# Optimization experiments

Hardware: AMD Instinct MI355X
Metric: run time of the kernel (lower is better)

The kernel has to match this reference:

```python
import jax, jax.numpy as jnp
import numpy as np

B, S, D, H, HID = 4, 2048, 1024, 16, 4096
DK = D // H
EPS = 1e-6


def layernorm(x, alpha, bias):
    # Matches the custom LayerNorm: std with Bessel correction (torch default),
    # and eps added to std (not variance).
    mean = jnp.mean(x, axis=-1, keepdims=True)
    std = jnp.std(x, axis=-1, ddof=1, keepdims=True)
    return alpha * (x - mean) / (std + EPS) + bias


def setup_inputs() -> dict:
    key = jax.random.key(0)
    ks = jax.random.split(key, 10)
    s = 0.02
    return {
        "x": jax.random.normal(ks[0], (B, S, D), dtype=jnp.float32),
        "wq": jax.random.normal(ks[1], (D, D), dtype=jnp.float32) * s,
        "wk": jax.random.normal(ks[2], (D, D), dtype=jnp.float32) * s,
        "wv": jax.random.normal(ks[3], (D, D), dtype=jnp.float32) * s,
        "wo": jax.random.normal(ks[4], (D, D), dtype=jnp.float32) * s,
        "w1": jax.random.normal(ks[5], (D, HID), dtype=jnp.float32) * s,
        "b1": jnp.zeros((HID,), dtype=jnp.float32),
        "w2": jax.random.normal(ks[6], (HID, D), dtype=jnp.float32) * s,
        "b2": jnp.zeros((D,), dtype=jnp.float32),
        "ln1_a": jnp.ones((D,), dtype=jnp.float32),
        "ln1_b": jnp.zeros((D,), dtype=jnp.float32),
        "ln2_a": jnp.ones((D,), dtype=jnp.float32),
        "ln2_b": jnp.zeros((D,), dtype=jnp.float32),
    }


def reference(x, wq, wk, wv, wo, w1, b1, w2, b2, ln1_a, ln1_b, ln2_a, ln2_b):
    # --- residual 1: pre-norm self-attention ---
    h = layernorm(x, ln1_a, ln1_b)
    q = (h @ wq).reshape(B, S, H, DK)
    k = (h @ wk).reshape(B, S, H, DK)
    v = (h @ wv).reshape(B, S, H, DK)
    scores = jnp.einsum("bqhd,bkhd->bhqk", q, k) / jnp.sqrt(jnp.float32(DK))
    # Faithful replication of the original mask: tril on a (1, max_len) matrix
    # keeps only key position 0; all other key positions get -1e9.
    key_keep = (jnp.arange(S) == 0)  # [S]
    scores = jnp.where(key_keep[None, None, None, :], scores, jnp.float32(-1e9))
    attn = jax.nn.softmax(scores, axis=-1)  # [B,H,S,S]
    ctx = jnp.einsum("bhqk,bkhd->bqhd", attn, v).reshape(B, S, D)
    x = x + ctx @ wo
    # --- residual 2: pre-norm FFN ---
    h2 = layernorm(x, ln2_a, ln2_b)
    ff = jax.nn.gelu(h2 @ w1 + b1, approximate=False) @ w2 + b2
    return x + ff
```

## Files before the change

kernel.cpp:

```cpp
#include <hip/hip_runtime.h>
#include <cstdint>

#define D_MODEL 1024
#define HIDDEN  4096
#define BATCH   4
#define SEQ     2048
#define NROWS   (BATCH*SEQ)

typedef __attribute__((ext_vector_type(4))) int i32x4;

#define ACT_AMAX 4.0f
#define ACT_S    (ACT_AMAX / 127.0f)
#define ACT_INV  (127.0f / ACT_AMAX)

#define GLDS16(g, l) __builtin_amdgcn_global_load_lds(                        \
    (const __attribute__((address_space(1))) unsigned int*)(g),               \
    (__attribute__((address_space(3))) unsigned int*)(l), 16, 0, 0)

__device__ __forceinline__ float block_sum(float v, float* s4) {
  #pragma unroll
  for (int off = 32; off > 0; off >>= 1) v += __shfl_down(v, off);
  int lane = threadIdx.x & 63, wid = threadIdx.x >> 6;
  __syncthreads();
  if (lane == 0) s4[wid] = v;
  __syncthreads();
  return s4[0] + s4[1] + s4[2] + s4[3];
}

__device__ __forceinline__ float block_max(float v, float* s4) {
  #pragma unroll
  for (int off = 32; off > 0; off >>= 1) v = fmaxf(v, __shfl_down(v, off));
  int lane = threadIdx.x & 63, wid = threadIdx.x >> 6;
  __syncthreads();
  if (lane == 0) s4[wid] = v;
  __syncthreads();
  return fmaxf(fmaxf(s4[0], s4[1]), fmaxf(s4[2], s4[3]));
}

__device__ __forceinline__ signed char qclamp(float v) {
  float r = rintf(v);
  r = fminf(127.f, fmaxf(-127.f, r));
  return (signed char)(int)r;
}

#define KCHUNKS 32
#define KCH     (D_MODEL / KCHUNKS)


__device__ __forceinline__ void absmax_cols_body(
    const float* __restrict__ in, int R, int C, unsigned* __restrict__ u,
    int bx, int by) {
  int c  = bx * 256 + threadIdx.x;
  int r0 = by * 64;
  float m = 0.f;
  #pragma unroll 4
  for (int r = 0; r < 64; ++r)
    m = fmaxf(m, fabsf(in[(size_t)(r0 + r) * C + c]));
  atomicMax(&u[c], __float_as_uint(m));
}

__device__ __forceinline__ void transpose_quant_body(
    const float* __restrict__ in, signed char* __restrict__ out,
    int R, int C, const unsigned* __restrict__ u,
    float (*tile)[33], int bx, int by) {
  int c0 = bx * 32, r0 = by * 32;
  int tx = threadIdx.x & 31, ty = threadIdx.x >> 5;
  #pragma unroll
  for (int i = ty; i < 32; i += 8)
    tile[i][tx] = in[(size_t)(r0 + i) * C + c0 + tx];
  __syncthreads();
  #pragma unroll
  for (int i = ty; i < 32; i += 8) {
    float f = __uint_as_float(u[c0 + i]);
    float inv = f > 0.f ? 127.f / f : 0.f;
    out[(size_t)(c0 + i) * R + r0 + tx] = qclamp(tile[tx][i] * inv);
  }
}

__device__ __forceinline__ void ln_matvec_body(
    const float* __restrict__ x, const float* __restrict__ ln_a,
    const float* __restrict__ ln_b, const float* __restrict__ W,
    float* __restrict__ vout, float* s4, float (*hs)[KCH], int bx, int by) {
  int n  = bx * 256 + threadIdx.x;
  int k0 = by * KCH;
  int t  = threadIdx.x;
  float4 g4 = ((const float4*)ln_a)[t];
  float4 b4 = ((const float4*)ln_b)[t];
  #pragma unroll
  for (int b = 0; b < 4; ++b) {
    const float* xr = x + (size_t)b * SEQ * D_MODEL;
    float4 v = ((const float4*)xr)[t];
    float sum = v.x + v.y + v.z + v.w;
    float mean = block_sum(sum, s4) * (1.f / 1024.f);
    float cx = v.x - mean, cy = v.y - mean, cz = v.z - mean, cw = v.w - mean;
    float sq = cx * cx + cy * cy + cz * cz + cw * cw;
    float var = block_sum(sq, s4) * (1.f / 1023.f);
    float inv = 1.f / (sqrtf(var) + 1e-6f);
    if (t >= (k0 >> 2) && t < ((k0 + KCH) >> 2)) {
      int lc = 4 * t - k0;
      hs[b][lc + 0] = g4.x * cx * inv + b4.x;
      hs[b][lc + 1] = g4.y * cy * inv + b4.y;
      hs[b][lc + 2] = g4.z * cz * inv + b4.z;
      hs[b][lc + 3] = g4.w * cw * inv + b4.w;
    }
  }
  __syncthreads();
  float a0 = 0, a1 = 0, a2 = 0, a3 = 0;
  #pragma unroll
  for (int k = 0; k < KCH; ++k) {
    float w = W[(size_t)(k0 + k) * D_MODEL + n];
    a0 = fmaf(hs[0][k], w, a0);
    a1 = fmaf(hs[1][k], w, a1);
    a2 = fmaf(hs[2][k], w, a2);
    a3 = fmaf(hs[3][k], w, a3);
  }
  atomicAdd(&vout[0 * D_MODEL + n], a0);
  atomicAdd(&vout[1 * D_MODEL + n], a1);
  atomicAdd(&vout[2 * D_MODEL + n], a2);
  atomicAdd(&vout[3 * D_MODEL + n], a3);
}

__device__ __forceinline__ void matvec_body(
    const float* __restrict__ vin, const float* __restrict__ W,
    float* __restrict__ vout, float (*hs)[KCH], int bx, int by) {
  int n  = bx * 256 + threadIdx.x;
  int k0 = by * KCH;
  if (threadIdx.x < 4 * KCH)
    hs[threadIdx.x / KCH][threadIdx.x % KCH] =
        vin[(threadIdx.x / KCH) * D_MODEL + k0 + (threadIdx.x % KCH)];
  __syncthreads();
  float a0 = 0, a1 = 0, a2 = 0, a3 = 0;
  #pragma unroll
  for (int k = 0; k < KCH; ++k) {
    float w = W[(size_t)(k0 + k) * D_MODEL + n];
    a0 = fmaf(hs[0][k], w, a0);
    a1 = fmaf(hs[1][k], w, a1);
    a2 = fmaf(hs[2][k], w, a2);
    a3 = fmaf(hs[3][k], w, a3);
  }
  atomicAdd(&vout[0 * D_MODEL + n], a0);
  atomicAdd(&vout[1 * D_MODEL + n], a1);
  atomicAdd(&vout[2 * D_MODEL + n], a2);
  atomicAdd(&vout[3 * D_MODEL + n], a3);
}

__global__ __launch_bounds__(256) void pre1(
    const float* __restrict__ w1, const float* __restrict__ w2,
    unsigned* __restrict__ u1, unsigned* __restrict__ u2,
    const float* __restrict__ x, const float* __restrict__ ln1a,
    const float* __restrict__ ln1b, const float* __restrict__ wv,
    float* __restrict__ v0) {
  __shared__ float s4[4];
  __shared__ float hs[4][KCH];
  int id = blockIdx.x;
  if (id < 256) {
    absmax_cols_body(w1, D_MODEL, HIDDEN, u1, id & 15, id >> 4);
  } else if (id < 512) {
    int r = id - 256;
    absmax_cols_body(w2, HIDDEN, D_MODEL, u2, r & 3, r >> 2);
  } else {
    int r = id - 512;
    ln_matvec_body(x, ln1a, ln1b, wv, v0, s4, hs, r & 3, r >> 2);
  }
}

__global__ __launch_bounds__(256) void pre2(
    const float* __restrict__ w1, const float* __restrict__ w2,
    const unsigned* __restrict__ u1, const unsigned* __restrict__ u2,
    signed char* __restrict__ w1t, signed char* __restrict__ w2t,
    const float* __restrict__ v0, const float* __restrict__ wo,
    float* __restrict__ delta) {
  __shared__ float tile[32][33];
  __shared__ float hs[4][KCH];
  int id = blockIdx.x;
  if (id < 4096) {
    transpose_quant_body(w1, w1t, D_MODEL, HIDDEN, u1, tile, id & 127, id >> 7);
  } else if (id < 8192) {
    int r = id - 4096;
    transpose_quant_body(w2, w2t, HIDDEN, D_MODEL, u2, tile, r & 31, r >> 5);
  } else {
    int r = id - 8192;
    matvec_body(v0, wo, delta, hs, r & 3, r >> 2);
  }
}

__global__ __launch_bounds__(256) void fused_res_ln_q(
    const float* __restrict__ x, const float* __restrict__ delta,
    const float* __restrict__ g, const float* __restrict__ be,
    float* __restrict__ x1_out, signed char* __restrict__ h2,
    float* __restrict__ hscale) {
  __shared__ float s4[4];
  int row = blockIdx.x;
  int b = row >> 11;
  int t = threadIdx.x;
  float4 v  = ((const float4*)(x + (size_t)row * D_MODEL))[t];
  float4 d4 = ((const float4*)(delta + (size_t)b * D_MODEL))[t];
  v.x += d4.x; v.y += d4.y; v.z += d4.z; v.w += d4.w;
  float sum = v.x + v.y + v.z + v.w;
  float mean = block_sum(sum, s4) * (1.f / 1024.f);
  float cx = v.x - mean, cy = v.y - mean, cz = v.z - mean, cw = v.w - mean;
  float sq = cx * cx + cy * cy + cz * cz + cw * cw;
  float var = block_sum(sq, s4) * (1.f / 1023.f);
  float inv = 1.f / (sqrtf(var) + 1e-6f);
  ((float4*)(x1_out + (size_t)row * D_MODEL))[t] = v;
  float4 g4 = ((const float4*)g)[t];
  float4 b4 = ((const float4*)be)[t];
  float h0v = g4.x * cx * inv + b4.x;
  float h1v = g4.y * cy * inv + b4.y;
  float h2v = g4.z * cz * inv + b4.z;
  float h3v = g4.w * cw * inv + b4.w;
  float am = fmaxf(fmaxf(fabsf(h0v), fabsf(h1v)), fmaxf(fabsf(h2v), fabsf(h3v)));
  float amax = block_max(am, s4);
  float qs = amax > 0.f ? 127.f / amax : 0.f;
  unsigned q = ((unsigned)(unsigned char)(int)qclamp(h0v * qs)) |
               ((unsigned)(unsigned char)(int)qclamp(h1v * qs) << 8) |
               ((unsigned)(unsigned char)(int)qclamp(h2v * qs) << 16) |
               ((unsigned)(unsigned char)(int)qclamp(h3v * qs) << 24);
  ((unsigned*)(h2 + (size_t)row * D_MODEL))[t] = q;
  if (t == 0) hscale[row] = amax * (1.f / 127.f);
}

__global__ __launch_bounds__(256, 3) void gemm1_k128(
    const signed char* __restrict__ A, const signed char* __restrict__ Bt,
    const float* __restrict__ rowS, const unsigned* __restrict__ colU,
    const float* __restrict__ bias, signed char* __restrict__ Cq,
    int M, int N, int K) {
  __shared__ signed char LA[128][128];
  __shared__ signed char LB[128][128];

  int GN  = N / 128;
  int CX  = (GN >= 16) ? 16 : (GN >> 1);
  int id  = blockIdx.x;
  int xcd = id & 7;
  int r   = id >> 3;
  int cby = xcd >> 1, cbx = xcd & 1;
  int lby = r / CX,   lbx = r % CX;
  int by  = cby * 16 + lby;
  int bx  = cbx * CX + lbx;
  int m0  = by * 128, n0 = bx * 128;
  int NT  = K / 128;

  int t = threadIdx.x;
  int wid = t >> 6, lane = t & 63;
  int wm = wid >> 1, wn = wid & 1;
  int lr = lane & 15, kg = lane >> 4;
  int swz = (lr & 7) << 4;

  int rS = t >> 3;
  int cS = ((t & 7) ^ (rS & 7)) * 16;
  const signed char* Ag = A  + (size_t)(m0 + rS) * K + cS;
  const signed char* Bg = Bt + (size_t)(n0 + rS) * K + cS;
  int ldsOff = wid * 1024;

#define G1_STG(T) do {                                                         \
    size_t ko_ = (size_t)(T) * 128;                                            \
    GLDS16(Ag + ko_,                  &LA[0][0] + ldsOff);                     \
    GLDS16(Ag + ko_ + (size_t)32 * K, &LA[0][0] + ldsOff + 4096);              \
    GLDS16(Ag + ko_ + (size_t)64 * K, &LA[0][0] + ldsOff + 8192);              \
    GLDS16(Ag + ko_ + (size_t)96 * K, &LA[0][0] + ldsOff + 12288);             \
    GLDS16(Bg + ko_,                  &LB[0][0] + ldsOff);                     \
    GLDS16(Bg + ko_ + (size_t)32 * K, &LB[0][0] + ldsOff + 4096);              \
    GLDS16(Bg + ko_ + (size_t)64 * K, &LB[0][0] + ldsOff + 8192);              \
    GLDS16(Bg + ko_ + (size_t)96 * K, &LB[0][0] + ldsOff + 12288);             \
  } while (0)

#define G1_RD() do {                                                           \
    _Pragma("unroll") for (int mi = 0; mi < 4; ++mi)                           \
    _Pragma("unroll") for (int kk = 0; kk < 2; ++kk)                           \
      a[mi][kk] = *(const i32x4*)                                              \
          &LA[wm * 64 + mi * 16 + lr][(kk * 64 + kg * 16) ^ swz];              \
    _Pragma("unroll") for (int ni = 0; ni < 4; ++ni)                           \
    _Pragma("unroll") for (int kk = 0; kk < 2; ++kk)                           \
      b[ni][kk] = *(const i32x4*)                                              \
          &LB[wn * 64 + ni * 16 + lr][(kk * 64 + kg * 16) ^ swz];              \
  } while (0)

#define G1_MM() do {                                                           \
    _Pragma("unroll") for (int mi = 0; mi < 4; ++mi)                           \
    _Pragma("unroll") for (int ni = 0; ni < 4; ++ni)                           \
    _Pragma("unroll") for (int kk = 0; kk < 2; ++kk)                           \
      acc[mi][ni] = __builtin_amdgcn_mfma_i32_16x16x64_i8(                     \
          a[mi][kk], b[ni][kk], acc[mi][ni], 0, 0, 0);                         \
  } while (0)

  i32x4 acc[4][4] = {};
  i32x4 a[4][2];
  i32x4 b[4][2];

  for (int tt = 0; tt < NT; ++tt) {
    G1_STG(tt);
    asm volatile("s_waitcnt vmcnt(0)" ::: "memory");
    __builtin_amdgcn_s_barrier();
    G1_RD();
    G1_MM();
    __builtin_amdgcn_s_barrier();
  }

  int orow = m0 + wm * 64;
  int ocol = n0 + wn * 64;
  #pragma unroll
  for (int mf = 0; mf < 4; ++mf) {
    #pragma unroll
    for (int nf = 0; nf < 4; ++nf) {
      int col = ocol + nf * 16 + lr;
      float cs = __uint_as_float(colU[col]) * (1.f / 127.f);
      float bz = bias[col];
      #pragma unroll
      for (int j = 0; j < 4; ++j) {
        int row = orow + mf * 16 + kg * 4 + j;
        float rs = rowS[row];
        float val = (float)acc[mf][nf][j] * rs * cs + bz;
        float u = val * (0.7978845608f + 0.0356774081f * val * val);
        float e = __expf(2.f * u);
        float th = 1.f - 2.f / (e + 1.f);
        val = 0.5f * val * (1.f + th);
        Cq[(size_t)row * N + col] = qclamp(val * ACT_INV);
      }
    }
  }
#undef G1_STG
#undef G1_RD
#undef G1_MM
}

__global__ __launch_bounds__(256, 2) void gemm2_k256(
    const signed char* __restrict__ A, const signed char* __restrict__ Bt,
    const unsigned* __restrict__ colU, const float* __restrict__ bias,
    float* __restrict__ Cf, int M, int N, int K) {
  __shared__ signed char LA[128][256];
  __shared__ signed char LB[128][256];

  int GN  = N / 128;
  int CX  = (GN >= 16) ? 16 : (GN >> 1);
  int id  = blockIdx.x;
  int xcd = id & 7;
  int r   = id >> 3;
  int cby = xcd >> 1, cbx = xcd & 1;
  int lby = r / CX,   lbx = r % CX;
  int by  = cby * 16 + lby;
  int bx  = cbx * CX + lbx;
  int m0  = by * 128, n0 = bx * 128;
  int NT  = K / 256;

  int t = threadIdx.x;
  int wid = t >> 6, lane = t & 63;
  int wm = wid >> 1, wn = wid & 1;
  int lr = lane & 15, kg = lane >> 4;
  int swz = (lr & 7) << 4;

  int rS = t >> 4;
  int cS = ((t & 15) ^ (rS & 7)) * 16;
  const signed char* Ag = A  + (size_t)(m0 + rS) * K + cS;
  const signed char* Bg = Bt + (size_t)(n0 + rS) * K + cS;
  int ldsOff = wid * 1024;

#define G2_STG(T) do {                                                         \
    size_t ko_ = (size_t)(T) * 256;                                            \
    _Pragma("unroll") for (int j = 0; j < 8; ++j)                              \
      GLDS16(Ag + ko_ + (size_t)(16 * j) * K,                                  \
             &LA[0][0] + ldsOff + j * 4096);                                   \
    _Pragma("unroll") for (int j = 0; j < 8; ++j)                              \
      GLDS16(Bg + ko_ + (size_t)(16 * j) * K,                                  \
             &LB[0][0] + ldsOff + j * 4096);                                   \
  } while (0)

#define G2_RD() do {                                                           \
    _Pragma("unroll") for (int mi = 0; mi < 4; ++mi)                           \
    _Pragma("unroll") for (int kk = 0; kk < 4; ++kk)                           \
      a[mi][kk] = *(const i32x4*)                                              \
          &LA[wm * 64 + mi * 16 + lr][(kk * 64 + kg * 16) ^ swz];              \
    _Pragma("unroll") for (int ni = 0; ni < 4; ++ni)                           \
    _Pragma("unroll") for (int kk = 0; kk < 4; ++kk)                           \
      b[ni][kk] = *(const i32x4*)                                              \
          &LB[wn * 64 + ni * 16 + lr][(kk * 64 + kg * 16) ^ swz];              \
  } while (0)

#define G2_MM() do {                                                           \
    _Pragma("unroll") for (int mi = 0; mi < 4; ++mi)                           \
    _Pragma("unroll") for (int ni = 0; ni < 4; ++ni)                           \
    _Pragma("unroll") for (int kk = 0; kk < 4; ++kk)                           \
      acc[mi][ni] = __builtin_amdgcn_mfma_i32_16x16x64_i8(                     \
          a[mi][kk], b[ni][kk], acc[mi][ni], 0, 0, 0);                         \
  } while (0)

  i32x4 acc[4][4] = {};
  i32x4 a[4][4];
  i32x4 b[4][4];

  for (int tt = 0; tt < NT; ++tt) {
    G2_STG(tt);
    asm volatile("s_waitcnt vmcnt(0)" ::: "memory");
    __builtin_amdgcn_s_barrier();
    G2_RD();
    G2_MM();
    __builtin_amdgcn_s_barrier();
  }

  int orow = m0 + wm * 64;
  int ocol = n0 + wn * 64;
  #pragma unroll
  for (int mf = 0; mf < 4; ++mf) {
    #pragma unroll
    for (int nf = 0; nf < 4; ++nf) {
      int col = ocol + nf * 16 + lr;
      float cs = __uint_as_float(colU[col]) * (1.f / 127.f);
      float bz = bias[col];
      #pragma unroll
      for (int j = 0; j < 4; ++j) {
        int row = orow + mf * 16 + kg * 4 + j;
        float val = (float)acc[mf][nf][j] * ACT_S * cs + bz;
        size_t idx = (size_t)row * N + col;
        Cf[idx] = Cf[idx] + val;
      }
    }
  }
#undef G2_STG
#undef G2_RD
#undef G2_MM
}

extern "C" void kernel_launch(void* const* d_in, const int* in_sizes, int n_in,
                              void* d_out, int out_size, void* d_ws, size_t ws_size,
                              hipStream_t stream) {
  const float* x    = (const float*)d_in[0];
  const float* wv   = (const float*)d_in[3];
  const float* wo   = (const float*)d_in[4];
  const float* w1   = (const float*)d_in[5];
  const float* b1   = (const float*)d_in[6];
  const float* w2   = (const float*)d_in[7];
  const float* b2   = (const float*)d_in[8];
  const float* ln1a = (const float*)d_in[9];
  const float* ln1b = (const float*)d_in[10];
  const float* ln2a = (const float*)d_in[11];
  const float* ln2b = (const float*)d_in[12];
  float* out = (float*)d_out;

  char* ws = (char*)d_ws;
  signed char* w1t = (signed char*)(ws);
  signed char* w2t = (signed char*)(ws + (4ull  << 20));
  signed char* h2  = (signed char*)(ws + (8ull  << 20));
  signed char* act = (signed char*)(ws + (16ull << 20));
  char* sc = ws + (48ull << 20);
  unsigned* u1    = (unsigned*)(sc);
  unsigned* u2    = (unsigned*)(sc + 16384);
  float*    v0    = (float*)(sc + 20480);
  float*    delta = (float*)(sc + 36864);
  float*    hsc   = (float*)(sc + 53248);

  hipMemsetAsync(sc, 0, 53248, stream);

  pre1<<<640, 256, 0, stream>>>(w1, w2, u1, u2, x, ln1a, ln1b, wv, v0);

  pre2<<<8320, 256, 0, stream>>>(w1, w2, u1, u2, w1t, w2t, v0, wo, delta);

  fused_res_ln_q<<<NROWS, 256, 0, stream>>>(x, delta, ln2a, ln2b, out, h2, hsc);

  gemm1_k128<<<(NROWS / 128) * (HIDDEN / 128), 256, 0, stream>>>(
      h2, w1t, hsc, u1, b1, act, NROWS, HIDDEN, D_MODEL);

  gemm2_k256<<<(NROWS / 128) * (D_MODEL / 128), 256, 0, stream>>>(
      act, w2t, u2, b2, out, NROWS, D_MODEL, HIDDEN);
}
```

Measured before the change: 167.6 us.

## Double-buffer LDS tiles in both int8 FFN GEMMs to overlap loads with MFMA

Both int8 GEMMs now hold two LDS stages and prefetch the next K tile with global_load_lds while MFMAs run on the current one. A partial vmcnt wait lets the newer loads stay in flight across the barrier. gemm2 drops its K tile from 256 to 128 so two stages fit in the same LDS footprint. gemm1's occupancy hint goes from 3 to 2 blocks per CU because its LDS use doubles, and the last iteration issues a redundant reload of the final tile.

```diff
diff --git a/kernel.cpp b/kernel.cpp
--- a/kernel.cpp
+++ b/kernel.cpp
@@ -220,13 +220,13 @@
   if (t == 0) hscale[row] = amax * (1.f / 127.f);
 }
 
-__global__ __launch_bounds__(256, 3) void gemm1_k128(
+__global__ __launch_bounds__(256, 2) void gemm1_t4(
     const signed char* __restrict__ A, const signed char* __restrict__ Bt,
     const float* __restrict__ rowS, const unsigned* __restrict__ colU,
     const float* __restrict__ bias, signed char* __restrict__ Cq,
     int M, int N, int K) {
-  __shared__ signed char LA[128][128];
-  __shared__ signed char LB[128][128];
+  __shared__ signed char LA[2][128][128];
+  __shared__ signed char LB[2][128][128];
 
   int GN  = N / 128;
   int CX  = (GN >= 16) ? 16 : (GN >> 1);
@@ -252,27 +252,27 @@
   const signed char* Bg = Bt + (size_t)(n0 + rS) * K + cS;
   int ldsOff = wid * 1024;
 
-#define G1_STG(T) do {                                                         \
+#define G1_STG(s, T) do {                                                      \
     size_t ko_ = (size_t)(T) * 128;                                            \
-    GLDS16(Ag + ko_,                  &LA[0][0] + ldsOff);                     \
-    GLDS16(Ag + ko_ + (size_t)32 * K, &LA[0][0] + ldsOff + 4096);              \
-    GLDS16(Ag + ko_ + (size_t)64 * K, &LA[0][0] + ldsOff + 8192);              \
-    GLDS16(Ag + ko_ + (size_t)96 * K, &LA[0][0] + ldsOff + 12288);             \
-    GLDS16(Bg + ko_,                  &LB[0][0] + ldsOff);                     \
-    GLDS16(Bg + ko_ + (size_t)32 * K, &LB[0][0] + ldsOff + 4096);              \
-    GLDS16(Bg + ko_ + (size_t)64 * K, &LB[0][0] + ldsOff + 8192);              \
-    GLDS16(Bg + ko_ + (size_t)96 * K, &LB[0][0] + ldsOff + 12288);             \
-  } while (0)
-
-#define G1_RD() do {                                                           \
+    GLDS16(Ag + ko_,                  &LA[s][0][0] + ldsOff);                  \
+    GLDS16(Ag + ko_ + (size_t)32 * K, &LA[s][0][0] + ldsOff + 4096);           \
+    GLDS16(Ag + ko_ + (size_t)64 * K, &LA[s][0][0] + ldsOff + 8192);           \
+    GLDS16(Ag + ko_ + (size_t)96 * K, &LA[s][0][0] + ldsOff + 12288);          \
+    GLDS16(Bg + ko_,                  &LB[s][0][0] + ldsOff);                  \
+    GLDS16(Bg + ko_ + (size_t)32 * K, &LB[s][0][0] + ldsOff + 4096);           \
+    GLDS16(Bg + ko_ + (size_t)64 * K, &LB[s][0][0] + ldsOff + 8192);           \
+    GLDS16(Bg + ko_ + (size_t)96 * K, &LB[s][0][0] + ldsOff + 12288);          \
+  } while (0)
+
+#define G1_RD(s) do {                                                          \
     _Pragma("unroll") for (int mi = 0; mi < 4; ++mi)                           \
     _Pragma("unroll") for (int kk = 0; kk < 2; ++kk)                           \
       a[mi][kk] = *(const i32x4*)                                              \
-          &LA[wm * 64 + mi * 16 + lr][(kk * 64 + kg * 16) ^ swz];              \
+          &LA[s][wm * 64 + mi * 16 + lr][(kk * 64 + kg * 16) ^ swz];           \
     _Pragma("unroll") for (int ni = 0; ni < 4; ++ni)                           \
     _Pragma("unroll") for (int kk = 0; kk < 2; ++kk)                           \
       b[ni][kk] = *(const i32x4*)                                              \
-          &LB[wn * 64 + ni * 16 + lr][(kk * 64 + kg * 16) ^ swz];              \
+          &LB[s][wn * 64 + ni * 16 + lr][(kk * 64 + kg * 16) ^ swz];           \
   } while (0)
 
 #define G1_MM() do {                                                           \
@@ -287,14 +287,18 @@
   i32x4 a[4][2];
   i32x4 b[4][2];
 
+  G1_STG(0, 0);
   for (int tt = 0; tt < NT; ++tt) {
-    G1_STG(tt);
-    asm volatile("s_waitcnt vmcnt(0)" ::: "memory");
+    int s = tt & 1;
+    int tn = tt + 1 < NT ? tt + 1 : NT - 1;
+    G1_STG(s ^ 1, tn);
+    asm volatile("s_waitcnt vmcnt(8)" ::: "memory");
     __builtin_amdgcn_s_barrier();
-    G1_RD();
+    G1_RD(s);
     G1_MM();
     __builtin_amdgcn_s_barrier();
   }
+  asm volatile("s_waitcnt vmcnt(0)" ::: "memory");
 
   int orow = m0 + wm * 64;
   int ocol = n0 + wn * 64;
@@ -323,12 +327,12 @@
 #undef G1_MM
 }
 
-__global__ __launch_bounds__(256, 2) void gemm2_k256(
+__global__ __launch_bounds__(256, 2) void gemm2_t4(
     const signed char* __restrict__ A, const signed char* __restrict__ Bt,
     const unsigned* __restrict__ colU, const float* __restrict__ bias,
     float* __restrict__ Cf, int M, int N, int K) {
-  __shared__ signed char LA[128][256];
-  __shared__ signed char LB[128][256];
+  __shared__ signed char LA[2][128][128];
+  __shared__ signed char LB[2][128][128];
 
   int GN  = N / 128;
   int CX  = (GN >= 16) ? 16 : (GN >> 1);
@@ -340,7 +344,7 @@
   int by  = cby * 16 + lby;
   int bx  = cbx * CX + lbx;
   int m0  = by * 128, n0 = bx * 128;
-  int NT  = K / 256;
+  int NT  = K / 128;
 
   int t = threadIdx.x;
   int wid = t >> 6, lane = t & 63;
@@ -348,53 +352,59 @@
   int lr = lane & 15, kg = lane >> 4;
   int swz = (lr & 7) << 4;
 
-  int rS = t >> 4;
-  int cS = ((t & 15) ^ (rS & 7)) * 16;
+  int rS = t >> 3;
+  int cS = ((t & 7) ^ (rS & 7)) * 16;
   const signed char* Ag = A  + (size_t)(m0 + rS) * K + cS;
   const signed char* Bg = Bt + (size_t)(n0 + rS) * K + cS;
   int ldsOff = wid * 1024;
 
-#define G2_STG(T) do {                                                         \
-    size_t ko_ = (size_t)(T) * 256;                                            \
-    _Pragma("unroll") for (int j = 0; j < 8; ++j)                              \
-      GLDS16(Ag + ko_ + (size_t)(16 * j) * K,                                  \
-             &LA[0][0] + ldsOff + j * 4096);                                   \
-    _Pragma("unroll") for (int j = 0; j < 8; ++j)                              \
-      GLDS16(Bg + ko_ + (size_t)(16 * j) * K,                                  \
-             &LB[0][0] + ldsOff + j * 4096);                                   \
-  } while (0)
-
-#define G2_RD() do {                                                           \
+#define G2_STG(s, T) do {                                                      \
+    size_t ko_ = (size_t)(T) * 128;                                            \
+    GLDS16(Ag + ko_,                  &LA[s][0][0] + ldsOff);                  \
+    GLDS16(Ag + ko_ + (size_t)32 * K, &LA[s][0][0] + ldsOff + 4096);           \
+    GLDS16(Ag + ko_ + (size_t)64 * K, &LA[s][0][0] + ldsOff + 8192);           \
+    GLDS16(Ag + ko_ + (size_t)96 * K, &LA[s][0][0] + ldsOff + 12288);          \
+    GLDS16(Bg + ko_,                  &LB[s][0][0] + ldsOff);                  \
+    GLDS16(Bg + ko_ + (size_t)32 * K, &LB[s][0][0] + ldsOff + 4096);           \
+    GLDS16(Bg + ko_ + (size_t)64 * K, &LB[s][0][0] + ldsOff + 8192);           \
+    GLDS16(Bg + ko_ + (size_t)96 * K, &LB[s][0][0] + ldsOff + 12288);          \
+  } while (0)
+
+#define G2_RD(s) do {                                                          \
     _Pragma("unroll") for (int mi = 0; mi < 4; ++mi)                           \
-    _Pragma("unroll") for (int kk = 0; kk < 4; ++kk)                           \
+    _Pragma("unroll") for (int kk = 0; kk < 2; ++kk)                           \
       a[mi][kk] = *(const i32x4*)                                              \
-          &LA[wm * 64 + mi * 16 + lr][(kk * 64 + kg * 16) ^ swz];              \
+          &LA[s][wm * 64 + mi * 16 + lr][(kk * 64 + kg * 16) ^ swz];           \
     _Pragma("unroll") for (int ni = 0; ni < 4; ++ni)                           \
-    _Pragma("unroll") for (int kk = 0; kk < 4; ++kk)                           \
+    _Pragma("unroll") for (int kk = 0; kk < 2; ++kk)                           \
       b[ni][kk] = *(const i32x4*)                                              \
-          &LB[wn * 64 + ni * 16 + lr][(kk * 64 + kg * 16) ^ swz];              \
+          &LB[s][wn * 64 + ni * 16 + lr][(kk * 64 + kg * 16) ^ swz];           \
   } while (0)
 
 #define G2_MM() do {                                                           \
     _Pragma("unroll") for (int mi = 0; mi < 4; ++mi)                           \
     _Pragma("unroll") for (int ni = 0; ni < 4; ++ni)                           \
-    _Pragma("unroll") for (int kk = 0; kk < 4; ++kk)                           \
+    _Pragma("unroll") for (int kk = 0; kk < 2; ++kk)                           \
       acc[mi][ni] = __builtin_amdgcn_mfma_i32_16x16x64_i8(                     \
           a[mi][kk], b[ni][kk], acc[mi][ni], 0, 0, 0);                         \
   } while (0)
 
   i32x4 acc[4][4] = {};
-  i32x4 a[4][4];
-  i32x4 b[4][4];
-
+  i32x4 a[4][2];
+  i32x4 b[4][2];
+
+  G2_STG(0, 0);
   for (int tt = 0; tt < NT; ++tt) {
-    G2_STG(tt);
-    asm volatile("s_waitcnt vmcnt(0)" ::: "memory");
+    int s = tt & 1;
+    int tn = tt + 1 < NT ? tt + 1 : NT - 1;
+    G2_STG(s ^ 1, tn);
+    asm volatile("s_waitcnt vmcnt(8)" ::: "memory");
     __builtin_amdgcn_s_barrier();
-    G2_RD();
+    G2_RD(s);
     G2_MM();
     __builtin_amdgcn_s_barrier();
   }
+  asm volatile("s_waitcnt vmcnt(0)" ::: "memory");
 
   int orow = m0 + wm * 64;
   int ocol = n0 + wn * 64;
@@ -455,9 +465,9 @@
 
   fused_res_ln_q<<<NROWS, 256, 0, stream>>>(x, delta, ln2a, ln2b, out, h2, hsc);
 
-  gemm1_k128<<<(NROWS / 128) * (HIDDEN / 128), 256, 0, stream>>>(
+  gemm1_t4<<<(NROWS / 128) * (HIDDEN / 128), 256, 0, stream>>>(
       h2, w1t, hsc, u1, b1, act, NROWS, HIDDEN, D_MODEL);
 
-  gemm2_k256<<<(NROWS / 128) * (D_MODEL / 128), 256, 0, stream>>>(
+  gemm2_t4<<<(NROWS / 128) * (D_MODEL / 128), 256, 0, stream>>>(
       act, w2t, u2, b2, out, NROWS, D_MODEL, HIDDEN);
 }
```

Measured after the change: 164.8 us. About the same (-1.7%).
